# Performance work log

Measured on AMD Instinct MI355X. Metric: run time of the kernel, lower is better.

## Reference

```python
import jax, jax.numpy as jnp
import numpy as np

STUDENT_TEMP = 0.1
CENTER_MOMENTUM = 0.9
N_CROPS = 8
GLOBAL_CROPS = 2
TOPK = 8
WARMUP_TEACHER_TEMP = 0.04
TEACHER_TEMP = 0.07
WARMUP_EPOCHS = 30
NEPOCHS = 100
B = 256          # per-crop batch
D = 8192         # out_dim


def setup_inputs() -> dict:
    key = jax.random.key(0)
    k1, k2, k3, k4 = jax.random.split(key, 4)
    return {
        "student_output": jax.random.normal(k1, (N_CROPS * B, D), jnp.float32),
        "teacher_output": jax.random.normal(k2, (GLOBAL_CROPS * B, D), jnp.float32),
        "predictor_table": 0.02 * jax.random.normal(k3, (D, D), jnp.float32),
        "center": 0.1 * jax.random.normal(k4, (1, D), jnp.float32),
        "epoch": 35,
    }


def reference(student_output, teacher_output, predictor_table, center, epoch):
    # teacher temperature schedule (static, epoch is a Python int)
    temps = np.concatenate([
        np.linspace(WARMUP_TEACHER_TEMP, TEACHER_TEMP, WARMUP_EPOCHS),
        np.ones(NEPOCHS - WARMUP_EPOCHS) * TEACHER_TEMP,
    ])
    temp = float(temps[epoch])

    # student/teacher softmaxes, chunked per crop
    student_probs = jax.nn.softmax(student_output / STUDENT_TEMP, axis=-1)
    s_chunks = jnp.split(student_probs, N_CROPS, axis=0)          # n_crops x [B, D]
    teacher_probs = jax.nn.softmax((teacher_output - center) / temp, axis=-1)
    t_chunks = jnp.split(teacher_probs, GLOBAL_CROPS, axis=0)     # global_crops x [B, D]

    # pairwise topk-weighted cross entropy
    total_loss = jnp.float32(0.0)
    n_loss_terms = 0
    for iq in range(GLOBAL_CROPS):
        for v in range(N_CROPS):
            if v <= iq:
                continue
            s = t_chunks[iq]                                       # [B, D] teacher probs
            f = s_chunks[v]                                        # [B, D] student probs
            p, indices = jax.lax.top_k(s, TOPK)                    # [B, K]
            p = p / jnp.sum(p, axis=-1, keepdims=True)
            pred = predictor_table[indices] / STUDENT_TEMP         # [B, K, D] gather
            logp = jax.nn.log_softmax(pred, axis=-1)               # [B, K, D]
            # -sum_k sum_d p[b,k] * f[b,d] * logp[b,k,d]  (outer-product weighting)
            loss_b = -jnp.einsum('bk,bd,bkd->b', p, f, logp)
            total_loss = total_loss + loss_b.mean()
            n_loss_terms += 1
    total_loss = total_loss / n_loss_terms

    # EMA center update (no-grad in original; world_size = 1)
    t_ng = jax.lax.stop_gradient(teacher_output)
    batch_center = jnp.mean(t_ng, axis=0, keepdims=True)           # [1, D]
    new_center = center * CENTER_MOMENTUM + batch_center * (1.0 - CENTER_MOMENTUM)

    log_sm_center = jax.nn.log_softmax(center, axis=-1)
    true_entropy = jnp.sum(jax.nn.softmax(center, axis=-1) * log_sm_center, axis=-1)
    entropy = jnp.sum(jax.nn.softmax(batch_center, axis=-1) * log_sm_center, axis=-1)

    return (total_loss, entropy, true_entropy, new_center)
```

## Files before the change

kernel.cpp:

```cpp
#include <hip/hip_runtime.h>
#include <hip/hip_bf16.h>
#include <math.h>

#define D 8192
#define NT 256

__device__ __forceinline__ float wave_sum(float v) {
    #pragma unroll
    for (int o = 32; o > 0; o >>= 1) v += __shfl_xor(v, o, 64);
    return v;
}

__global__ __launch_bounds__(NT) void k_topk4(
    const float* __restrict__ teacher, const float* __restrict__ center,
    float* __restrict__ cand_v, int* __restrict__ cand_i, float* __restrict__ out)
{
    const int bid = blockIdx.x;
    const int row = bid >> 2;
    const int ch  = bid & 3;
    const int t = threadIdx.x;
    const int lane = t & 63, w = t >> 6;
    __shared__ float svv[8][4];
    __shared__ int   sii[8][4];

    if (bid == 0 && t == 0) out[0] = 0.f;

    const float* trow = teacher + (size_t)row * D + ch * 2048;
    const float* crow = center + ch * 2048;
    float z[8];
    {
        float4 tv0 = *(const float4*)(trow + t * 4);
        float4 cv0 = *(const float4*)(crow + t * 4);
        float4 tv1 = *(const float4*)(trow + 1024 + t * 4);
        float4 cv1 = *(const float4*)(crow + 1024 + t * 4);
        z[0] = tv0.x - cv0.x; z[1] = tv0.y - cv0.y; z[2] = tv0.z - cv0.z; z[3] = tv0.w - cv0.w;
        z[4] = tv1.x - cv1.x; z[5] = tv1.y - cv1.y; z[6] = tv1.z - cv1.z; z[7] = tv1.w - cv1.w;
    }

    float mvl = -INFINITY; int mjl = 0;
    #pragma unroll
    for (int j = 0; j < 8; ++j)
        if (z[j] > mvl) { mvl = z[j]; mjl = j; }

    float topv[8]; int topc[8];
    #pragma unroll 1
    for (int k = 0; k < 8; ++k) {
        float mv = mvl;
        int mc = (t << 3) | mjl;
        #pragma unroll
        for (int o = 32; o > 0; o >>= 1) {
            float ov = __shfl_xor(mv, o, 64);
            int   oc = __shfl_xor(mc, o, 64);
            if (ov > mv) { mv = ov; mc = oc; }
        }
        if (lane == 0) { svv[k][w] = mv; sii[k][w] = mc; }
        __syncthreads();
        float gv = svv[k][0]; int gc = sii[k][0];
        #pragma unroll
        for (int j = 1; j < 4; ++j)
            if (svv[k][j] > gv) { gv = svv[k][j]; gc = sii[k][j]; }
        topv[k] = gv; topc[k] = gc;
        if ((gc >> 3) == t) {
            z[gc & 7] = -INFINITY;
            mvl = -INFINITY; mjl = 0;
            #pragma unroll
            for (int j = 0; j < 8; ++j)
                if (z[j] > mvl) { mvl = z[j]; mjl = j; }
        }
    }

    if (t == 0) {
        #pragma unroll
        for (int k = 0; k < 8; ++k) {
            const int q = topc[k] >> 3, j = topc[k] & 7;
            const int col = ch * 2048 + ((j < 4) ? (q * 4 + j) : (1024 + q * 4 + (j - 4)));
            cand_v[(size_t)row * 32 + ch * 8 + k] = topv[k];
            cand_i[(size_t)row * 32 + ch * 8 + k] = col;
        }
    }
}

__global__ __launch_bounds__(NT) void k_gather(
    const float* __restrict__ pred, const float* __restrict__ cand_v,
    const int* __restrict__ cand_i, const int* __restrict__ epoch_p,
    const float* __restrict__ teacher,
    float* __restrict__ g_ws, float* __restrict__ part_lse,
    float* __restrict__ p_ws, float* __restrict__ part)
{
    const int bid = blockIdx.x;
    const int t = threadIdx.x;

    if (bid >= 2048) {
        const int cb = bid - 2048;
        const int rc = cb >> 3, dc = cb & 7;
        const int d0 = dc * 1024 + t * 4;
        const float* base = teacher + (size_t)rc * 32 * D + d0;
        float4 acc = make_float4(0.f, 0.f, 0.f, 0.f);
        #pragma unroll 4
        for (int r = 0; r < 32; ++r) {
            float4 x = *(const float4*)(base + (size_t)r * D);
            acc.x += x.x; acc.y += x.y; acc.z += x.z; acc.w += x.w;
        }
        *(float4*)(part + (size_t)rc * D + d0) = acc;
        return;
    }

    const int row = bid >> 2;
    const int ch  = bid & 3;
    const int lane = t & 63, w = t >> 6;
    const int d0 = ch * 2048 + t * 4;
    __shared__ float sred[4][8];

    float cv[32]; int ci[32];
    #pragma unroll
    for (int k = 0; k < 32; ++k) {
        cv[k] = cand_v[(size_t)row * 32 + k];
        ci[k] = cand_i[(size_t)row * 32 + k];
    }
    float tv[8]; int jk[8];
    #pragma unroll
    for (int k = 0; k < 8; ++k) {
        float mv = cv[0]; int mi = 0;
        #pragma unroll
        for (int j = 1; j < 32; ++j)
            if (cv[j] > mv) { mv = cv[j]; mi = j; }
        tv[k] = mv; jk[k] = ci[mi]; cv[mi] = -INFINITY;
    }

    const int e = epoch_p[0];
    const float temp = (e < 30) ? (0.04f + 0.03f * (float)e / 29.0f) : 0.07f;
    float pk[8]; float norm = 0.f;
    #pragma unroll
    for (int k = 0; k < 8; ++k) { pk[k] = __expf((tv[k] - tv[0]) / temp); norm += pk[k]; }
    const float invn = 1.0f / norm;
    #pragma unroll
    for (int k = 0; k < 8; ++k) pk[k] *= invn;

    if (ch == 0 && t < 8) p_ws[row * 8 + t] = pk[t];

    float4 a0 = make_float4(0.f,0.f,0.f,0.f), a1 = make_float4(0.f,0.f,0.f,0.f);
    float se[8];
    #pragma unroll
    for (int k = 0; k < 8; ++k) {
        const float* prow = pred + (size_t)jk[k] * D;
        float4 x0 = *(const float4*)(prow + d0);
        float4 x1 = *(const float4*)(prow + d0 + 1024);
        se[k] = __expf(x0.x*10.f) + __expf(x0.y*10.f) + __expf(x0.z*10.f) + __expf(x0.w*10.f)
              + __expf(x1.x*10.f) + __expf(x1.y*10.f) + __expf(x1.z*10.f) + __expf(x1.w*10.f);
        const float p = pk[k];
        a0.x += p*x0.x; a0.y += p*x0.y; a0.z += p*x0.z; a0.w += p*x0.w;
        a1.x += p*x1.x; a1.y += p*x1.y; a1.z += p*x1.z; a1.w += p*x1.w;
    }
    float* grow = g_ws + (size_t)row * D;
    *(float4*)(grow + d0)        = a0;
    *(float4*)(grow + d0 + 1024) = a1;

    #pragma unroll
    for (int k = 0; k < 8; ++k) se[k] = wave_sum(se[k]);
    if (lane == 0) {
        #pragma unroll
        for (int k = 0; k < 8; ++k) sred[w][k] = se[k];
    }
    __syncthreads();
    if (t < 8)
        part_lse[(size_t)bid * 8 + t] =
            sred[0][t] + sred[1][t] + sred[2][t] + sred[3][t];
}

__global__ __launch_bounds__(NT) void k_main(
    const float* __restrict__ student, const float* __restrict__ g_ws,
    const float* __restrict__ p_ws, const float* __restrict__ part_lse,
    const float* __restrict__ part, const float* __restrict__ center,
    float* __restrict__ out)
{
    const int bid = blockIdx.x;
    const int t = threadIdx.x;
    const int lane = t & 63, w = t >> 6;

    if (bid < 2) {
        __shared__ float sm4[4];
        const int r = (bid << 8) | t;
        float c = 0.f;
        #pragma unroll
        for (int k = 0; k < 8; ++k) {
            float s = part_lse[(size_t)(r*4+0)*8+k] + part_lse[(size_t)(r*4+1)*8+k]
                    + part_lse[(size_t)(r*4+2)*8+k] + part_lse[(size_t)(r*4+3)*8+k];
            c += p_ws[r * 8 + k] * __logf(s);
        }
        const float wgt = (bid == 0) ? 7.0f : 6.0f;
        float vv = wave_sum(c * wgt * (1.0f / 3328.0f));
        if (lane == 0) sm4[w] = vv;
        __syncthreads();
        if (t == 0) atomicAdd(out, sm4[0] + sm4[1] + sm4[2] + sm4[3]);
        return;
    }

    if (bid == 2) {
        __shared__ float sm4[4];
        float c[32], bc[32];
        #pragma unroll
        for (int i = 0; i < 8; ++i) {
            const int d = i * 1024 + t * 4;
            float4 cv = *(const float4*)(center + d);
            float4 s = make_float4(0.f, 0.f, 0.f, 0.f);
            for (int rc = 0; rc < 16; ++rc) {
                float4 p = *(const float4*)(part + (size_t)rc * D + d);
                s.x += p.x; s.y += p.y; s.z += p.z; s.w += p.w;
            }
            const float sc = 1.0f / 512.0f;
            bc[i*4+0] = s.x * sc; bc[i*4+1] = s.y * sc;
            bc[i*4+2] = s.z * sc; bc[i*4+3] = s.w * sc;
            c[i*4+0] = cv.x; c[i*4+1] = cv.y; c[i*4+2] = cv.z; c[i*4+3] = cv.w;
            out[3 + d + 0] = cv.x * 0.9f + bc[i*4+0] * 0.1f;
            out[3 + d + 1] = cv.y * 0.9f + bc[i*4+1] * 0.1f;
            out[3 + d + 2] = cv.z * 0.9f + bc[i*4+2] * 0.1f;
            out[3 + d + 3] = cv.w * 0.9f + bc[i*4+3] * 0.1f;
        }

        float mc = -INFINITY, mb = -INFINITY;
        #pragma unroll
        for (int i = 0; i < 32; ++i) { mc = fmaxf(mc, c[i]); mb = fmaxf(mb, bc[i]); }
        #pragma unroll
        for (int o = 32; o > 0; o >>= 1) {
            mc = fmaxf(mc, __shfl_xor(mc, o, 64));
            mb = fmaxf(mb, __shfl_xor(mb, o, 64));
        }
        if (lane == 0) sm4[w] = mc;
        __syncthreads();
        mc = fmaxf(fmaxf(sm4[0], sm4[1]), fmaxf(sm4[2], sm4[3]));
        __syncthreads();
        if (lane == 0) sm4[w] = mb;
        __syncthreads();
        mb = fmaxf(fmaxf(sm4[0], sm4[1]), fmaxf(sm4[2], sm4[3]));
        __syncthreads();

        float zc = 0.f, zb = 0.f;
        #pragma unroll
        for (int i = 0; i < 32; ++i) { zc += __expf(c[i] - mc); zb += __expf(bc[i] - mb); }
        zc = wave_sum(zc); zb = wave_sum(zb);
        if (lane == 0) sm4[w] = zc;
        __syncthreads();
        zc = sm4[0] + sm4[1] + sm4[2] + sm4[3];
        __syncthreads();
        if (lane == 0) sm4[w] = zb;
        __syncthreads();
        zb = sm4[0] + sm4[1] + sm4[2] + sm4[3];
        __syncthreads();
        const float lnZc = __logf(zc);

        float te = 0.f, en = 0.f;
        #pragma unroll
        for (int i = 0; i < 32; ++i) {
            const float lsm = c[i] - mc - lnZc;
            te += __expf(c[i] - mc) * lsm;
            en += __expf(bc[i] - mb) * lsm;
        }
        te = wave_sum(te); en = wave_sum(en);
        if (lane == 0) sm4[w] = te;
        __syncthreads();
        te = sm4[0] + sm4[1] + sm4[2] + sm4[3];
        __syncthreads();
        if (lane == 0) sm4[w] = en;
        __syncthreads();
        en = sm4[0] + sm4[1] + sm4[2] + sm4[3];
        if (t == 0) {
            out[1] = en / zb;
            out[2] = te / zc;
        }
        return;
    }

    __shared__ float sred3[4][3];
    const int row = 256 + (bid - 3);
    const int v = row >> 8;
    const int b = row & 255;

    float y[32];
    const float* srow = student + (size_t)row * D;
    #pragma unroll
    for (int i = 0; i < 8; ++i) {
        float4 x = *(const float4*)(srow + i * 1024 + t * 4);
        y[i*4+0] = __expf(x.x * 10.f); y[i*4+1] = __expf(x.y * 10.f);
        y[i*4+2] = __expf(x.z * 10.f); y[i*4+3] = __expf(x.w * 10.f);
    }
    float zs = 0.f;
    #pragma unroll
    for (int i = 0; i < 32; ++i) zs += y[i];

    const float* g0 = g_ws + (size_t)b * D;
    const float* g1 = g_ws + (size_t)(256 + b) * D;
    float a0 = 0.f, a1 = 0.f;
    #pragma unroll
    for (int i = 0; i < 8; ++i) {
        float4 gg = *(const float4*)(g0 + i * 1024 + t * 4);
        a0 += y[i*4+0]*gg.x + y[i*4+1]*gg.y + y[i*4+2]*gg.z + y[i*4+3]*gg.w;
    }
    if (v >= 2) {
        #pragma unroll
        for (int i = 0; i < 8; ++i) {
            float4 gg = *(const float4*)(g1 + i * 1024 + t * 4);
            a1 += y[i*4+0]*gg.x + y[i*4+1]*gg.y + y[i*4+2]*gg.z + y[i*4+3]*gg.w;
        }
    }
    zs = wave_sum(zs); a0 = wave_sum(a0); a1 = wave_sum(a1);
    if (lane == 0) { sred3[w][0] = zs; sred3[w][1] = a0; sred3[w][2] = a1; }
    __syncthreads();
    if (t == 0) {
        const float Z  = sred3[0][0] + sred3[1][0] + sred3[2][0] + sred3[3][0];
        const float A0 = sred3[0][1] + sred3[1][1] + sred3[2][1] + sred3[3][1];
        const float A1 = sred3[0][2] + sred3[1][2] + sred3[2][2] + sred3[3][2];
        const float invZ = 1.0f / Z;
        float term = -10.f * A0 * invZ;
        if (v >= 2) term += -10.f * A1 * invZ;
        atomicAdd(out, term * (1.0f / 3328.0f));
    }
}

extern "C" void kernel_launch(void* const* d_in, const int* in_sizes, int n_in,
                              void* d_out, int out_size, void* d_ws, size_t ws_size,
                              hipStream_t stream) {
    const float* student = (const float*)d_in[0];
    const float* teacher = (const float*)d_in[1];
    const float* pred    = (const float*)d_in[2];
    const float* center  = (const float*)d_in[3];
    const int*   epoch   = (const int*)d_in[4];
    float* out = (float*)d_out;

    float* g_ws     = (float*)d_ws;
    float* part     = g_ws + (size_t)512 * D;
    float* p_ws     = part + (size_t)16 * D;
    float* part_lse = p_ws + 512 * 8;
    float* cand_v   = part_lse + 2048 * 8;
    int*   cand_i   = (int*)(cand_v + 512 * 32);

    k_topk4<<<2048, NT, 0, stream>>>(teacher, center, cand_v, cand_i, out);
    k_gather<<<2176, NT, 0, stream>>>(pred, cand_v, cand_i, epoch, teacher,
                                      g_ws, part_lse, p_ws, part);
    k_main<<<1795, NT, 0, stream>>>(student, g_ws, p_ws, part_lse, part, center, out);
}
```

Measured before the change: 82.19 us.

## Fuse top-k and predictor gather into one 1024-thread kernel per teacher row

Merges the per-chunk top-k kernel and the gather/log-sum-exp kernel into a single kernel where one 1024-thread block handles a whole teacher row. The candidate merge step and workspace round trip go away, and the per-row LSE term is reduced and atomically accumulated in the same block, which removes two small reduction blocks from the main kernel. The column-sum partials are regrouped to 32 chunks of 16 rows, and the output is zeroed with a memset. Removing one launch is traded against lower block parallelism (544 blocks instead of 2048+) and longer top-k reductions across 16 waves.

```diff
diff --git a/kernel.cpp b/kernel.cpp
--- a/kernel.cpp
+++ b/kernel.cpp
@@ -3,7 +3,6 @@
 #include <math.h>
 
 #define D 8192
-#define NT 256
 
 __device__ __forceinline__ float wave_sum(float v) {
     #pragma unroll
@@ -11,28 +10,45 @@
     return v;
 }
 
-__global__ __launch_bounds__(NT) void k_topk4(
+__global__ __launch_bounds__(1024) void k_fused(
     const float* __restrict__ teacher, const float* __restrict__ center,
-    float* __restrict__ cand_v, int* __restrict__ cand_i, float* __restrict__ out)
+    const float* __restrict__ pred, const int* __restrict__ epoch_p,
+    float* __restrict__ g_ws, float* __restrict__ part, float* __restrict__ out)
 {
     const int bid = blockIdx.x;
-    const int row = bid >> 2;
-    const int ch  = bid & 3;
     const int t = threadIdx.x;
+
+    if (bid >= 512) {
+        const int cb = bid - 512;
+        const int d0 = t * 4, d1 = 4096 + t * 4;
+        const float* base = teacher + (size_t)cb * 16 * D;
+        float4 a0 = make_float4(0.f,0.f,0.f,0.f), a1 = make_float4(0.f,0.f,0.f,0.f);
+        #pragma unroll 4
+        for (int r = 0; r < 16; ++r) {
+            float4 x0 = *(const float4*)(base + (size_t)r * D + d0);
+            float4 x1 = *(const float4*)(base + (size_t)r * D + d1);
+            a0.x += x0.x; a0.y += x0.y; a0.z += x0.z; a0.w += x0.w;
+            a1.x += x1.x; a1.y += x1.y; a1.z += x1.z; a1.w += x1.w;
+        }
+        *(float4*)(part + (size_t)cb * D + d0) = a0;
+        *(float4*)(part + (size_t)cb * D + d1) = a1;
+        return;
+    }
+
+    const int row = bid;
     const int lane = t & 63, w = t >> 6;
-    __shared__ float svv[8][4];
-    __shared__ int   sii[8][4];
-
-    if (bid == 0 && t == 0) out[0] = 0.f;
-
-    const float* trow = teacher + (size_t)row * D + ch * 2048;
-    const float* crow = center + ch * 2048;
+    __shared__ float svv[8][16];
+    __shared__ int   sii[8][16];
+    __shared__ float sred[16][8];
+
+    const float* trow = teacher + (size_t)row * D;
+    const int d0 = t * 4, d1 = 4096 + t * 4;
     float z[8];
     {
-        float4 tv0 = *(const float4*)(trow + t * 4);
-        float4 cv0 = *(const float4*)(crow + t * 4);
-        float4 tv1 = *(const float4*)(trow + 1024 + t * 4);
-        float4 cv1 = *(const float4*)(crow + 1024 + t * 4);
+        float4 tv0 = *(const float4*)(trow + d0);
+        float4 cv0 = *(const float4*)(center + d0);
+        float4 tv1 = *(const float4*)(trow + d1);
+        float4 cv1 = *(const float4*)(center + d1);
         z[0] = tv0.x - cv0.x; z[1] = tv0.y - cv0.y; z[2] = tv0.z - cv0.z; z[3] = tv0.w - cv0.w;
         z[4] = tv1.x - cv1.x; z[5] = tv1.y - cv1.y; z[6] = tv1.z - cv1.z; z[7] = tv1.w - cv1.w;
     }
@@ -57,7 +73,7 @@
         __syncthreads();
         float gv = svv[k][0]; int gc = sii[k][0];
         #pragma unroll
-        for (int j = 1; j < 4; ++j)
+        for (int j = 1; j < 16; ++j)
             if (svv[k][j] > gv) { gv = svv[k][j]; gc = sii[k][j]; }
         topv[k] = gv; topc[k] = gc;
         if ((gc >> 3) == t) {
@@ -69,74 +85,20 @@
         }
     }
 
-    if (t == 0) {
-        #pragma unroll
-        for (int k = 0; k < 8; ++k) {
-            const int q = topc[k] >> 3, j = topc[k] & 7;
-            const int col = ch * 2048 + ((j < 4) ? (q * 4 + j) : (1024 + q * 4 + (j - 4)));
-            cand_v[(size_t)row * 32 + ch * 8 + k] = topv[k];
-            cand_i[(size_t)row * 32 + ch * 8 + k] = col;
-        }
-    }
-}
-
-__global__ __launch_bounds__(NT) void k_gather(
-    const float* __restrict__ pred, const float* __restrict__ cand_v,
-    const int* __restrict__ cand_i, const int* __restrict__ epoch_p,
-    const float* __restrict__ teacher,
-    float* __restrict__ g_ws, float* __restrict__ part_lse,
-    float* __restrict__ p_ws, float* __restrict__ part)
-{
-    const int bid = blockIdx.x;
-    const int t = threadIdx.x;
-
-    if (bid >= 2048) {
-        const int cb = bid - 2048;
-        const int rc = cb >> 3, dc = cb & 7;
-        const int d0 = dc * 1024 + t * 4;
-        const float* base = teacher + (size_t)rc * 32 * D + d0;
-        float4 acc = make_float4(0.f, 0.f, 0.f, 0.f);
-        #pragma unroll 4
-        for (int r = 0; r < 32; ++r) {
-            float4 x = *(const float4*)(base + (size_t)r * D);
-            acc.x += x.x; acc.y += x.y; acc.z += x.z; acc.w += x.w;
-        }
-        *(float4*)(part + (size_t)rc * D + d0) = acc;
-        return;
-    }
-
-    const int row = bid >> 2;
-    const int ch  = bid & 3;
-    const int lane = t & 63, w = t >> 6;
-    const int d0 = ch * 2048 + t * 4;
-    __shared__ float sred[4][8];
-
-    float cv[32]; int ci[32];
-    #pragma unroll
-    for (int k = 0; k < 32; ++k) {
-        cv[k] = cand_v[(size_t)row * 32 + k];
-        ci[k] = cand_i[(size_t)row * 32 + k];
-    }
-    float tv[8]; int jk[8];
-    #pragma unroll
-    for (int k = 0; k < 8; ++k) {
-        float mv = cv[0]; int mi = 0;
-        #pragma unroll
-        for (int j = 1; j < 32; ++j)
-            if (cv[j] > mv) { mv = cv[j]; mi = j; }
-        tv[k] = mv; jk[k] = ci[mi]; cv[mi] = -INFINITY;
-    }
-
     const int e = epoch_p[0];
     const float temp = (e < 30) ? (0.04f + 0.03f * (float)e / 29.0f) : 0.07f;
-    float pk[8]; float norm = 0.f;
-    #pragma unroll
-    for (int k = 0; k < 8; ++k) { pk[k] = __expf((tv[k] - tv[0]) / temp); norm += pk[k]; }
+    float pk[8]; int jk[8];
+    float norm = 0.f;
+    #pragma unroll
+    for (int k = 0; k < 8; ++k) {
+        const int to = topc[k] >> 3, j = topc[k] & 7;
+        jk[k] = (j < 4) ? (to * 4 + j) : (4096 + to * 4 + (j - 4));
+        pk[k] = __expf((topv[k] - topv[0]) / temp);
+        norm += pk[k];
+    }
     const float invn = 1.0f / norm;
     #pragma unroll
     for (int k = 0; k < 8; ++k) pk[k] *= invn;
-
-    if (ch == 0 && t < 8) p_ws[row * 8 + t] = pk[t];
 
     float4 a0 = make_float4(0.f,0.f,0.f,0.f), a1 = make_float4(0.f,0.f,0.f,0.f);
     float se[8];
@@ -144,7 +106,7 @@
     for (int k = 0; k < 8; ++k) {
         const float* prow = pred + (size_t)jk[k] * D;
         float4 x0 = *(const float4*)(prow + d0);
-        float4 x1 = *(const float4*)(prow + d0 + 1024);
+        float4 x1 = *(const float4*)(prow + d1);
         se[k] = __expf(x0.x*10.f) + __expf(x0.y*10.f) + __expf(x0.z*10.f) + __expf(x0.w*10.f)
               + __expf(x1.x*10.f) + __expf(x1.y*10.f) + __expf(x1.z*10.f) + __expf(x1.w*10.f);
         const float p = pk[k];
@@ -152,8 +114,8 @@
         a1.x += p*x1.x; a1.y += p*x1.y; a1.z += p*x1.z; a1.w += p*x1.w;
     }
     float* grow = g_ws + (size_t)row * D;
-    *(float4*)(grow + d0)        = a0;
-    *(float4*)(grow + d0 + 1024) = a1;
+    *(float4*)(grow + d0) = a0;
+    *(float4*)(grow + d1) = a1;
 
     #pragma unroll
     for (int k = 0; k < 8; ++k) se[k] = wave_sum(se[k]);
@@ -162,14 +124,22 @@
         for (int k = 0; k < 8; ++k) sred[w][k] = se[k];
     }
     __syncthreads();
-    if (t < 8)
-        part_lse[(size_t)bid * 8 + t] =
-            sred[0][t] + sred[1][t] + sred[2][t] + sred[3][t];
-}
-
-__global__ __launch_bounds__(NT) void k_main(
+    if (t == 0) {
+        float c = 0.f;
+        #pragma unroll
+        for (int k = 0; k < 8; ++k) {
+            float S = 0.f;
+            #pragma unroll
+            for (int j = 0; j < 16; ++j) S += sred[j][k];
+            c += pk[k] * __logf(S);
+        }
+        const float wgt = (row < 256) ? 7.0f : 6.0f;
+        atomicAdd(out, c * wgt * (1.0f / 3328.0f));
+    }
+}
+
+__global__ __launch_bounds__(256) void k_main(
     const float* __restrict__ student, const float* __restrict__ g_ws,
-    const float* __restrict__ p_ws, const float* __restrict__ part_lse,
     const float* __restrict__ part, const float* __restrict__ center,
     float* __restrict__ out)
 {
@@ -177,25 +147,7 @@
     const int t = threadIdx.x;
     const int lane = t & 63, w = t >> 6;
 
-    if (bid < 2) {
-        __shared__ float sm4[4];
-        const int r = (bid << 8) | t;
-        float c = 0.f;
-        #pragma unroll
-        for (int k = 0; k < 8; ++k) {
-            float s = part_lse[(size_t)(r*4+0)*8+k] + part_lse[(size_t)(r*4+1)*8+k]
-                    + part_lse[(size_t)(r*4+2)*8+k] + part_lse[(size_t)(r*4+3)*8+k];
-            c += p_ws[r * 8 + k] * __logf(s);
-        }
-        const float wgt = (bid == 0) ? 7.0f : 6.0f;
-        float vv = wave_sum(c * wgt * (1.0f / 3328.0f));
-        if (lane == 0) sm4[w] = vv;
-        __syncthreads();
-        if (t == 0) atomicAdd(out, sm4[0] + sm4[1] + sm4[2] + sm4[3]);
-        return;
-    }
-
-    if (bid == 2) {
+    if (bid == 0) {
         __shared__ float sm4[4];
         float c[32], bc[32];
         #pragma unroll
@@ -203,7 +155,7 @@
             const int d = i * 1024 + t * 4;
             float4 cv = *(const float4*)(center + d);
             float4 s = make_float4(0.f, 0.f, 0.f, 0.f);
-            for (int rc = 0; rc < 16; ++rc) {
+            for (int rc = 0; rc < 32; ++rc) {
                 float4 p = *(const float4*)(part + (size_t)rc * D + d);
                 s.x += p.x; s.y += p.y; s.z += p.z; s.w += p.w;
             }
@@ -271,7 +223,7 @@
     }
 
     __shared__ float sred3[4][3];
-    const int row = 256 + (bid - 3);
+    const int row = 255 + bid;
     const int v = row >> 8;
     const int b = row & 255;
 
@@ -326,15 +278,11 @@
     const int*   epoch   = (const int*)d_in[4];
     float* out = (float*)d_out;
 
-    float* g_ws     = (float*)d_ws;
-    float* part     = g_ws + (size_t)512 * D;
-    float* p_ws     = part + (size_t)16 * D;
-    float* part_lse = p_ws + 512 * 8;
-    float* cand_v   = part_lse + 2048 * 8;
-    int*   cand_i   = (int*)(cand_v + 512 * 32);
-
-    k_topk4<<<2048, NT, 0, stream>>>(teacher, center, cand_v, cand_i, out);
-    k_gather<<<2176, NT, 0, stream>>>(pred, cand_v, cand_i, epoch, teacher,
-                                      g_ws, part_lse, p_ws, part);
-    k_main<<<1795, NT, 0, stream>>>(student, g_ws, p_ws, part_lse, part, center, out);
-}
+    float* g_ws = (float*)d_ws;
+    float* part = g_ws + (size_t)512 * D;
+
+    hipMemsetAsync(d_out, 0, sizeof(float), stream);
+
+    k_fused<<<544, 1024, 0, stream>>>(teacher, center, pred, epoch, g_ws, part, out);
+    k_main<<<1793, 256, 0, stream>>>(student, g_ws, part, center, out);
+}
```

Measured after the change: 116.6 us. 41.9% more time.

## Split top-k merge into wave-parallel kernel and stabilize student softmax with max

Applied to the files above, without the earlier changes.

The 32-candidate top-8 merge and the softmax weight computation move out of the gather kernel into a small separate kernel. It uses one wavefront per row with shuffle-based argmax, so each of the 2048 gather blocks no longer repeats the serial 32x8 scan in every thread. The cost is an extra kernel launch and a workspace round trip. Separately, the student softmax now subtracts a block-wide row max before exponentiating, which adds a reduction and a barrier but avoids overflow of exp(10x).

```diff
diff --git a/kernel.cpp b/kernel.cpp
--- a/kernel.cpp
+++ b/kernel.cpp
@@ -80,12 +80,52 @@
     }
 }
 
-__global__ __launch_bounds__(NT) void k_gather(
-    const float* __restrict__ pred, const float* __restrict__ cand_v,
-    const int* __restrict__ cand_i, const int* __restrict__ epoch_p,
-    const float* __restrict__ teacher,
-    float* __restrict__ g_ws, float* __restrict__ part_lse,
-    float* __restrict__ p_ws, float* __restrict__ part)
+__global__ __launch_bounds__(NT) void k_merge(
+    const float* __restrict__ cand_v, const int* __restrict__ cand_i,
+    const int* __restrict__ epoch_p,
+    int* __restrict__ idx_ws, float* __restrict__ p_ws)
+{
+    const int t = threadIdx.x;
+    const int lane = t & 63, w = t >> 6;
+    const int row = blockIdx.x * 4 + w;
+
+    float v = (lane < 32) ? cand_v[(size_t)row * 32 + lane] : -INFINITY;
+    int   idx = (lane < 32) ? cand_i[(size_t)row * 32 + lane] : 0;
+    int payload = (idx << 6) | lane;
+
+    float topv[8]; int topi[8];
+    #pragma unroll
+    for (int k = 0; k < 8; ++k) {
+        float mv = v; int mp = payload;
+        #pragma unroll
+        for (int o = 32; o > 0; o >>= 1) {
+            float ov = __shfl_xor(mv, o, 64);
+            int   op = __shfl_xor(mp, o, 64);
+            if (ov > mv) { mv = ov; mp = op; }
+        }
+        topv[k] = mv; topi[k] = mp >> 6;
+        if (lane == (mp & 63)) v = -INFINITY;
+    }
+
+    if (lane == 0) {
+        const int e = epoch_p[0];
+        const float temp = (e < 30) ? (0.04f + 0.03f * (float)e / 29.0f) : 0.07f;
+        float wgt[8]; float norm = 0.f;
+        #pragma unroll
+        for (int k = 0; k < 8; ++k) { wgt[k] = __expf((topv[k] - topv[0]) / temp); norm += wgt[k]; }
+        const float invn = 1.0f / norm;
+        #pragma unroll
+        for (int k = 0; k < 8; ++k) {
+            p_ws[row * 8 + k] = wgt[k] * invn;
+            idx_ws[row * 8 + k] = topi[k];
+        }
+    }
+}
+
+__global__ __launch_bounds__(NT) void k_gather_colsum(
+    const float* __restrict__ pred, const int* __restrict__ idx_ws,
+    const float* __restrict__ p_ws, const float* __restrict__ teacher,
+    float* __restrict__ g_ws, float* __restrict__ part_lse, float* __restrict__ part)
 {
     const int bid = blockIdx.x;
     const int t = threadIdx.x;
@@ -111,32 +151,12 @@
     const int d0 = ch * 2048 + t * 4;
     __shared__ float sred[4][8];
 
-    float cv[32]; int ci[32];
-    #pragma unroll
-    for (int k = 0; k < 32; ++k) {
-        cv[k] = cand_v[(size_t)row * 32 + k];
-        ci[k] = cand_i[(size_t)row * 32 + k];
-    }
-    float tv[8]; int jk[8];
+    int jk[8]; float pk[8];
     #pragma unroll
     for (int k = 0; k < 8; ++k) {
-        float mv = cv[0]; int mi = 0;
-        #pragma unroll
-        for (int j = 1; j < 32; ++j)
-            if (cv[j] > mv) { mv = cv[j]; mi = j; }
-        tv[k] = mv; jk[k] = ci[mi]; cv[mi] = -INFINITY;
-    }
-
-    const int e = epoch_p[0];
-    const float temp = (e < 30) ? (0.04f + 0.03f * (float)e / 29.0f) : 0.07f;
-    float pk[8]; float norm = 0.f;
-    #pragma unroll
-    for (int k = 0; k < 8; ++k) { pk[k] = __expf((tv[k] - tv[0]) / temp); norm += pk[k]; }
-    const float invn = 1.0f / norm;
-    #pragma unroll
-    for (int k = 0; k < 8; ++k) pk[k] *= invn;
-
-    if (ch == 0 && t < 8) p_ws[row * 8 + t] = pk[t];
+        jk[k] = idx_ws[row * 8 + k];
+        pk[k] = p_ws[row * 8 + k];
+    }
 
     float4 a0 = make_float4(0.f,0.f,0.f,0.f), a1 = make_float4(0.f,0.f,0.f,0.f);
     float se[8];
@@ -270,6 +290,7 @@
         return;
     }
 
+    __shared__ float smax[4];
     __shared__ float sred3[4][3];
     const int row = 256 + (bid - 3);
     const int v = row >> 8;
@@ -277,15 +298,23 @@
 
     float y[32];
     const float* srow = student + (size_t)row * D;
+    float m = -INFINITY;
     #pragma unroll
     for (int i = 0; i < 8; ++i) {
         float4 x = *(const float4*)(srow + i * 1024 + t * 4);
-        y[i*4+0] = __expf(x.x * 10.f); y[i*4+1] = __expf(x.y * 10.f);
-        y[i*4+2] = __expf(x.z * 10.f); y[i*4+3] = __expf(x.w * 10.f);
-    }
+        y[i*4+0] = x.x * 10.f; y[i*4+1] = x.y * 10.f;
+        y[i*4+2] = x.z * 10.f; y[i*4+3] = x.w * 10.f;
+        m = fmaxf(m, fmaxf(fmaxf(y[i*4+0], y[i*4+1]), fmaxf(y[i*4+2], y[i*4+3])));
+    }
+    #pragma unroll
+    for (int o = 32; o > 0; o >>= 1) m = fmaxf(m, __shfl_xor(m, o, 64));
+    if (lane == 0) smax[w] = m;
+    __syncthreads();
+    const float M = fmaxf(fmaxf(smax[0], smax[1]), fmaxf(smax[2], smax[3]));
+
     float zs = 0.f;
     #pragma unroll
-    for (int i = 0; i < 32; ++i) zs += y[i];
+    for (int i = 0; i < 32; ++i) { y[i] = __expf(y[i] - M); zs += y[i]; }
 
     const float* g0 = g_ws + (size_t)b * D;
     const float* g1 = g_ws + (size_t)(256 + b) * D;
@@ -328,13 +357,15 @@
 
     float* g_ws     = (float*)d_ws;
     float* part     = g_ws + (size_t)512 * D;
-    float* p_ws     = part + (size_t)16 * D;
+    int*   idx_ws   = (int*)(part + (size_t)16 * D);
+    float* p_ws     = (float*)(idx_ws + 512 * 8);
     float* part_lse = p_ws + 512 * 8;
     float* cand_v   = part_lse + 2048 * 8;
     int*   cand_i   = (int*)(cand_v + 512 * 32);
 
     k_topk4<<<2048, NT, 0, stream>>>(teacher, center, cand_v, cand_i, out);
-    k_gather<<<2176, NT, 0, stream>>>(pred, cand_v, cand_i, epoch, teacher,
-                                      g_ws, part_lse, p_ws, part);
+    k_merge<<<128, NT, 0, stream>>>(cand_v, cand_i, epoch, idx_ws, p_ws);
+    k_gather_colsum<<<2176, NT, 0, stream>>>(pred, idx_ws, p_ws, teacher,
+                                             g_ws, part_lse, part);
     k_main<<<1795, NT, 0, stream>>>(student, g_ws, p_ws, part_lse, part, center, out);
 }
```

Result: faster. 79.11 us (-3.7%).
